# Optimization experiments

Hardware: AMD Instinct MI355X
Metric: run time of the kernel (lower is better)

The kernel has to match this reference:

```python
import jax, jax.numpy as jnp
import numpy as np

K_SIZE = 7
D_MODEL = 128
D_Q = 64
N_HEADS = 4
D_FF = 512
EPS = 1e-5


def _windows(x, k):
    # x: [N,E,H,W] -> [N,E,P,H,W]; zero-padded local k x k windows,
    # row-major over (dy,dx), matching nn.Unfold ordering.
    p = k // 2
    N, E, H, W = x.shape
    xp = jnp.pad(x, ((0, 0), (0, 0), (p, p), (p, p)))
    ws = [xp[:, :, i:i + H, j:j + W] for i in range(k) for j in range(k)]
    return jnp.stack(ws, axis=2)


def _layernorm(x, g, b):
    m = jnp.mean(x, -1, keepdims=True)
    v = jnp.var(x, -1, keepdims=True)
    return (x - m) * jax.lax.rsqrt(v + EPS) * g + b


def setup_inputs() -> dict:
    key = jax.random.key(0)
    ks = jax.random.split(key, 12)
    E, Q, F = D_MODEL, D_Q, D_FF

    def g(k, shape, s=0.02):
        return jax.random.normal(k, shape, jnp.float32) * s

    return dict(
        x=jax.random.normal(ks[0], (4, E, 64, 64), jnp.float32),
        qcoeff=jax.random.normal(ks[1], (4, Q), jnp.float32),
        wq=g(ks[2], (E, E)), bq=jnp.zeros((E,), jnp.float32),
        wk=g(ks[3], (E, E)), bk=jnp.zeros((E,), jnp.float32),
        wv=g(ks[4], (E, E)), bv=jnp.zeros((E,), jnp.float32),
        rel_bias=jnp.zeros((N_HEADS, K_SIZE * K_SIZE), jnp.float32),
        ln1_g=jnp.ones((E,), jnp.float32), ln1_b=jnp.zeros((E,), jnp.float32),
        bil_w=g(ks[5], (E, E, Q)), bil_b=jnp.zeros((E,), jnp.float32),
        ln2_g=jnp.ones((E,), jnp.float32), ln2_b=jnp.zeros((E,), jnp.float32),
        w1=g(ks[6], (F, E)), b1=jnp.zeros((F,), jnp.float32),
        w2=g(ks[7], (E, F)), b2=jnp.zeros((E,), jnp.float32),
    )


def reference(x, qcoeff, wq, bq, wk, bk, wv, bv, rel_bias, ln1_g, ln1_b,
              bil_w, bil_b, ln2_g, ln2_b, w1, b1, w2, b2):
    N, E, H, W = x.shape
    Nh = N_HEADS
    Hd = E // Nh
    P = K_SIZE * K_SIZE

    x_nhwc = jnp.transpose(x, (0, 2, 3, 1))              # [N,H,W,E]
    xn = _layernorm(x_nhwc, ln1_g, ln1_b)
    xnc = jnp.transpose(xn, (0, 3, 1, 2))                # [N,E,H,W]

    # 1x1-conv projections
    q = jnp.einsum('nchw,oc->nohw', xnc, wq) + bq[None, :, None, None]
    k = jnp.einsum('nchw,oc->nohw', xnc, wk) + bk[None, :, None, None]
    v = jnp.einsum('nchw,oc->nohw', xnc, wv) + bv[None, :, None, None]

    # local windows of K/V: [N,Nh,Hd,P,H,W]
    Kw = _windows(k, K_SIZE).reshape(N, Nh, Hd, P, H, W)
    Vw = _windows(v, K_SIZE).reshape(N, Nh, Hd, P, H, W)
    Qh = q.reshape(N, Nh, Hd, H, W)

    scores = jnp.einsum('nhdyx,nhdpyx->nhpyx', Qh, Kw)
    scores = scores + rel_bias[None, :, :, None, None]
    attn = jax.nn.softmax(scores, axis=2)                # softmax over P
    out = jnp.einsum('nhpyx,nhdpyx->nhdyx', attn, Vw).reshape(N, E, H, W)
    z0 = jnp.transpose(out, (0, 2, 3, 1))                # [N,H,W,E]

    # Bilinear(z0, qcoeff): qcoeff constant per (H,W) -> contract once per batch
    t = jnp.einsum('oiq,nq->noi', bil_w, qcoeff)         # [N,E,E]
    z1 = jnp.einsum('nhwi,noi->nhwo', z0, t) + bil_b

    z2 = z1 + x_nhwc
    z3 = _layernorm(z2, ln2_g, ln2_b)
    h1 = jax.nn.gelu(z3 @ w1.T + b1, approximate=False)  # dropout inactive (eval)
    z4 = h1 @ w2.T + b2 + z2
    return jnp.transpose(z4, (0, 3, 1, 2))               # [N,E,H,W]
```

## Files before the change

### kernel.cpp

```cpp
#include <hip/hip_runtime.h>
#include <cmath>

#define EPS 1e-5f
#define SZ 2097152

typedef __attribute__((ext_vector_type(8))) short short8;
typedef __attribute__((ext_vector_type(4))) float floatx4;

__device__ __forceinline__ float dot4(float4 a, float4 b) {
  return fmaf(a.x, b.x, fmaf(a.y, b.y, fmaf(a.z, b.z, a.w * b.w)));
}

__device__ __forceinline__ short f2bf(float f) {
  union { float f; unsigned u; } v; v.f = f;
  unsigned r = v.u + 0x7fff + ((v.u >> 16) & 1);
  return (short)(r >> 16);
}

#define MFMA16(a, b, c) __builtin_amdgcn_mfma_f32_16x16x32_bf16(a, b, c, 0, 0, 0)

__global__ __launch_bounds__(256) void k_prep(const float* __restrict__ w1,
    const float* __restrict__ w2, const float* __restrict__ wq,
    const float* __restrict__ wk, const float* __restrict__ wv,
    const float* __restrict__ bil_w, const float* __restrict__ qcoeff,
    short* __restrict__ w1bf, short* __restrict__ w2bf,
    short* __restrict__ wqbf, short* __restrict__ wkbf, short* __restrict__ wvbf,
    short* __restrict__ tb) {
  __shared__ float qs[256];
  int tid = threadIdx.x;
  qs[tid] = qcoeff[tid];
  __syncthreads();
  int tid0 = blockIdx.x * 256 + tid;
  int stride = gridDim.x * 256;
  for (int i = tid0; i < 16384; i += stride) {
    int flat = i * 4; int f = flat >> 7, c = flat & 127;
    float4 v = *(const float4*)&w1[flat];
    short t4[4] = {f2bf(v.x), f2bf(v.y), f2bf(v.z), f2bf(v.w)};
    *(uint2*)&w1bf[f * 136 + c] = *(uint2*)t4;
  }
  for (int i = tid0; i < 16384; i += stride) {
    int flat = i * 4; int o = flat >> 9, j = flat & 511;
    int ck = j >> 7, jj = j & 127;
    float4 v = *(const float4*)&w2[flat];
    short t4[4] = {f2bf(v.x), f2bf(v.y), f2bf(v.z), f2bf(v.w)};
    *(uint2*)&w2bf[(ck * 128 + o) * 136 + jj] = *(uint2*)t4;
  }
  for (int i = tid0; i < 4096; i += stride) {
    int flat = i * 4; int o = flat >> 7, c = flat & 127;
    float4 a = *(const float4*)&wq[flat];
    float4 b = *(const float4*)&wk[flat];
    float4 cc = *(const float4*)&wv[flat];
    short ta[4] = {f2bf(a.x), f2bf(a.y), f2bf(a.z), f2bf(a.w)};
    short tb4[4] = {f2bf(b.x), f2bf(b.y), f2bf(b.z), f2bf(b.w)};
    short tc[4] = {f2bf(cc.x), f2bf(cc.y), f2bf(cc.z), f2bf(cc.w)};
    *(uint2*)&wqbf[o * 136 + c] = *(uint2*)ta;
    *(uint2*)&wkbf[o * 136 + c] = *(uint2*)tb4;
    *(uint2*)&wvbf[o * 136 + c] = *(uint2*)tc;
  }
  {
    int flat = tid0;
    const float* wrow = bil_w + (size_t)flat * 64;
    float acc[4] = {0.f, 0.f, 0.f, 0.f};
    for (int qq = 0; qq < 64; qq += 4) {
      float4 w4 = *(const float4*)&wrow[qq];
#pragma unroll
      for (int nn = 0; nn < 4; ++nn) {
        const float* qc = &qs[nn * 64 + qq];
        acc[nn] = fmaf(w4.x, qc[0], fmaf(w4.y, qc[1], fmaf(w4.z, qc[2], fmaf(w4.w, qc[3], acc[nn]))));
      }
    }
    int o = flat >> 7, i = flat & 127;
#pragma unroll
    for (int nn = 0; nn < 4; ++nn) tb[nn * 17408 + o * 136 + i] = f2bf(acc[nn]);
  }
}

__global__ __launch_bounds__(512) void k_qkvln(const float* __restrict__ x,
    const float* __restrict__ g, const float* __restrict__ b,
    const short* __restrict__ wqbf, const short* __restrict__ wkbf,
    const short* __restrict__ wvbf, const float* __restrict__ bq,
    const float* __restrict__ bk, const float* __restrict__ bv,
    float* __restrict__ xnhwc, short* __restrict__ qbf,
    short* __restrict__ kbf, short* __restrict__ vtb) {
  __shared__ float tile[128 * 33];
  __shared__ float mres[32], rres[32];
  __shared__ __align__(16) short xs[32 * 136];
  int tid = threadIdx.x;
  int bid = blockIdx.x;
  int half = bid & 1, ny = bid >> 1;
  int n = ny >> 6, y = ny & 63;
  const float* xb = x + (size_t)n * 524288 + y * 64 + half * 32;
  for (int it = 0; it < 8; ++it) {
    int flat = it * 512 + tid;
    int c = flat >> 5, xpl = flat & 31;
    tile[c * 33 + xpl] = xb[(size_t)c * 4096 + xpl];
  }
  __syncthreads();
  {
    int pxl = tid >> 4, cl = tid & 15;
    float s = 0.f, sq = 0.f;
#pragma unroll
    for (int j = 0; j < 8; ++j) {
      float v = tile[(cl * 8 + j) * 33 + pxl];
      s += v; sq += v * v;
    }
    s += __shfl_xor(s, 1);  sq += __shfl_xor(sq, 1);
    s += __shfl_xor(s, 2);  sq += __shfl_xor(sq, 2);
    s += __shfl_xor(s, 4);  sq += __shfl_xor(sq, 4);
    s += __shfl_xor(s, 8);  sq += __shfl_xor(sq, 8);
    if (cl == 0) {
      float m = s * (1.f / 128.f);
      float var = sq * (1.f / 128.f) - m * m;
      mres[pxl] = m;
      rres[pxl] = rsqrtf(var + EPS);
    }
  }
  __syncthreads();
  size_t rowbase = (size_t)ny * 8192 + half * 4096;
  for (int it = 0; it < 8; ++it) {
    int flat = it * 512 + tid;
    int c = flat & 127, pxl = flat >> 7;
    float v = tile[c * 33 + pxl];
    xnhwc[rowbase + flat] = v;
    xs[pxl * 136 + c] = f2bf((v - mres[pxl]) * rres[pxl] * g[c] + b[c]);
  }
  __syncthreads();
  int w = tid >> 6, lane = tid & 63;
  int quad = lane >> 4, r16 = lane & 15;
  int wm = w & 1, wn = w >> 1;
  int stripl = wm * 16;
  short8 a[4];
#pragma unroll
  for (int kk = 0; kk < 4; ++kk)
    a[kk] = *(const short8*)&xs[(stripl + r16) * 136 + kk * 32 + quad * 8];
  const short* wptr[3] = {wqbf, wkbf, wvbf};
  const float* bptr[3] = {bq, bk, bv};
  for (int m = 0; m < 3; ++m) {
    const short* wp = wptr[m];
    const float* bb = bptr[m];
#pragma unroll
    for (int nt = 0; nt < 2; ++nt) {
      int o0 = wn * 32 + nt * 16;
      floatx4 acc = {0.f, 0.f, 0.f, 0.f};
#pragma unroll
      for (int kk = 0; kk < 4; ++kk) {
        short8 bfr = *(const short8*)&wp[(o0 + r16) * 136 + kk * 32 + quad * 8];
        acc = MFMA16(a[kk], bfr, acc);
      }
      float bv2 = bb[o0 + r16];
      if (m < 2) {
        short* dst = (m == 0) ? qbf : kbf;
#pragma unroll
        for (int r = 0; r < 4; ++r) {
          int pxl = stripl + quad * 4 + r;
          dst[rowbase + pxl * 128 + o0 + r16] = f2bf(acc[r] + bv2);
        }
      } else {
        short t4[4] = {f2bf(acc[0] + bv2), f2bf(acc[1] + bv2),
                       f2bf(acc[2] + bv2), f2bf(acc[3] + bv2)};
        *(uint2*)&vtb[(size_t)(n * 128 + o0 + r16) * 4096 + y * 64 + half * 32 +
                      stripl + quad * 4] = *(uint2*)t4;
      }
    }
  }
}

__global__ __launch_bounds__(256) void k_attn(const short* __restrict__ qbf,
    const short* __restrict__ kbf, const short* __restrict__ vtb,
    const float* __restrict__ rel_bias, float* __restrict__ z0) {
  __shared__ float ssf[4][16 * 50];
  __shared__ __align__(16) short AbB[4][16 * 68];
  __shared__ float biasS[4][52];
  int bid = blockIdx.x;
  int h = bid & 3, y = (bid >> 2) & 63, n = bid >> 8;
  int tid = threadIdx.x;
  int w = tid >> 6, lane = tid & 63;
  int quad = lane >> 4, r16 = lane & 15;
  int strip = w * 16;
  float* ssfw = ssf[w];
  short* Abw = AbB[w];
  float* biasw = biasS[w];
  {
    unsigned* ad = (unsigned*)Abw;
    for (int i = lane; i < 544; i += 64) ad[i] = 0u;
  }
  if (lane < 49) biasw[lane] = rel_bias[h * 49 + lane];
  const short* qrow = qbf + (size_t)n * 524288 + (size_t)y * 64 * 128 + h * 32;
  short8 qf = *(const short8*)&qrow[(strip + r16) * 128 + quad * 8];
  const short* kbp = kbf + (size_t)n * 524288 + h * 32;
#pragma unroll
  for (int r = 0; r < 7; ++r) {
    int yy = y + r - 3;
    bool yok = (unsigned)yy < 64u;
    int yyc = min(max(yy, 0), 63);
#pragma unroll
    for (int t = 0; t < 2; ++t) {
      int xxc = (w + t) * 16 + r16;
      int gx = xxc - 3;
      bool ok = yok && ((unsigned)gx < 64u);
      int gxc = min(max(gx, 0), 63);
      short8 bf = *(const short8*)&kbp[(size_t)(yyc * 64 + gxc) * 128 + quad * 8];
      floatx4 c = MFMA16(qf, bf, ((floatx4){0.f, 0.f, 0.f, 0.f}));
#pragma unroll
      for (int rr = 0; rr < 4; ++rr) {
        int lrow = quad * 4 + rr;
        int dx = xxc - (strip + lrow);
        if ((unsigned)dx < 7u) {
          float val = ok ? c[rr] : 0.f;
          ssfw[lrow * 50 + r * 7 + dx] = val + biasw[r * 7 + dx];
        }
      }
    }
  }
  {
    int lrow = lane >> 2, sub = lane & 3;
    int p0 = sub * 12, cnt = (sub == 3) ? 13 : 12;
    float sv[13];
    float mx = -1e30f;
    for (int pi = 0; pi < cnt; ++pi) { sv[pi] = ssfw[lrow * 50 + p0 + pi]; mx = fmaxf(mx, sv[pi]); }
    mx = fmaxf(mx, __shfl_xor(mx, 1));
    mx = fmaxf(mx, __shfl_xor(mx, 2));
    float sum = 0.f;
    for (int pi = 0; pi < cnt; ++pi) { float e = __expf(sv[pi] - mx); sv[pi] = e; sum += e; }
    sum += __shfl_xor(sum, 1);
    sum += __shfl_xor(sum, 2);
    float inv = 1.f / sum;
    for (int pi = 0; pi < cnt; ++pi) ssfw[lrow * 50 + p0 + pi] = sv[pi] * inv;
  }
  floatx4 oacc[2] = {(floatx4){0.f, 0.f, 0.f, 0.f}, (floatx4){0.f, 0.f, 0.f, 0.f}};
  int kk0 = (w == 3) ? 1 : 0;
  int kk1 = (w == 0) ? 0 : 1;
  int lrow = lane >> 2, sub = lane & 3;
  int pxg = strip + lrow;
  const short* vbp = vtb + (size_t)(n * 128 + h * 32) * 4096;
  for (int r = 0; r < 7; ++r) {
    int yy = y + r - 3;
    bool yok = (unsigned)yy < 64u;
    int yyc = min(max(yy, 0), 63);
    int c0 = pxg + sub - 3;
    if ((unsigned)c0 < 64u) Abw[lrow * 68 + c0] = f2bf(ssfw[lrow * 50 + r * 7 + sub]);
    int c1 = pxg + sub + 1;
    if (sub < 3 && (unsigned)c1 < 64u)
      Abw[lrow * 68 + c1] = f2bf(ssfw[lrow * 50 + r * 7 + sub + 4]);
    for (int kk = kk0; kk <= kk1; ++kk) {
      short8 af = *(const short8*)&Abw[r16 * 68 + kk * 32 + quad * 8];
#pragma unroll
      for (int nt = 0; nt < 2; ++nt) {
        short8 vf = *(const short8*)&vbp[(size_t)(nt * 16 + r16) * 4096 + yyc * 64 + kk * 32 + quad * 8];
        if (!yok) vf = (short8){0, 0, 0, 0, 0, 0, 0, 0};
        oacc[nt] = MFMA16(af, vf, oacc[nt]);
      }
    }
  }
  float* zrow = z0 + (size_t)n * 524288 + (size_t)y * 64 * 128 + h * 32;
#pragma unroll
  for (int nt = 0; nt < 2; ++nt)
#pragma unroll
    for (int rr = 0; rr < 4; ++rr) {
      int px = strip + quad * 4 + rr;
      zrow[px * 128 + nt * 16 + r16] = oacc[nt][rr];
    }
}

__global__ __launch_bounds__(512) void k_tail(const float* __restrict__ z0,
    const short* __restrict__ tb, const float* __restrict__ bil_b,
    const float* __restrict__ xnhwc, const float* __restrict__ g2,
    const float* __restrict__ b2ln, const short* __restrict__ w1bf,
    const float* __restrict__ b1, const short* __restrict__ w2bf,
    const float* __restrict__ b2, float* __restrict__ out) {
  __shared__ __align__(16) char smem[8704 + 8704 + 16896];
  short* z3s = (short*)smem;
  short* h1s = (short*)(smem + 8704);
  float* z2s = (float*)(smem + 17408);
  float* outt = (float*)smem;
  int tid = threadIdx.x;
  int bid = blockIdx.x;
  int half = bid & 1, ny = bid >> 1;
  int n = ny >> 6, y = ny & 63;
  size_t rowbase = (size_t)ny * 8192 + half * 4096;
  for (int it = 0; it < 2; ++it) {
    int flat = (it * 512 + tid) * 4;
    int pxl = flat >> 7, c = flat & 127;
    float4 v = *(const float4*)&z0[rowbase + flat];
    short tmp[4] = {f2bf(v.x), f2bf(v.y), f2bf(v.z), f2bf(v.w)};
    *(uint2*)&z3s[pxl * 136 + c] = *(uint2*)tmp;
  }
  __syncthreads();
  int w = tid >> 6, lane = tid & 63;
  int quad = lane >> 4, r16 = lane & 15;
  int wm = w & 1, wn = w >> 1;
  int stripl = wm * 16;
  {
    const short* tn = tb + (size_t)n * 17408;
    short8 a[4];
#pragma unroll
    for (int kk = 0; kk < 4; ++kk)
      a[kk] = *(const short8*)&z3s[(stripl + r16) * 136 + kk * 32 + quad * 8];
#pragma unroll
    for (int nt = 0; nt < 2; ++nt) {
      int o0 = wn * 32 + nt * 16;
      floatx4 acc = {0.f, 0.f, 0.f, 0.f};
#pragma unroll
      for (int kk = 0; kk < 4; ++kk) {
        short8 bfr = *(const short8*)&tn[(o0 + r16) * 136 + kk * 32 + quad * 8];
        acc = MFMA16(a[kk], bfr, acc);
      }
      float bb = bil_b[o0 + r16];
#pragma unroll
      for (int r = 0; r < 4; ++r) {
        int pxl = stripl + quad * 4 + r;
        z2s[pxl * 132 + o0 + r16] = acc[r] + bb + xnhwc[rowbase + pxl * 128 + o0 + r16];
      }
    }
  }
  __syncthreads();
  {
    int pxl = tid >> 4, cl = tid & 15;
    float4 v0 = *(const float4*)&z2s[pxl * 132 + cl * 8];
    float4 v1 = *(const float4*)&z2s[pxl * 132 + cl * 8 + 4];
    float s = v0.x + v0.y + v0.z + v0.w + v1.x + v1.y + v1.z + v1.w;
    float sq = dot4(v0, v0) + dot4(v1, v1);
    s += __shfl_xor(s, 1);  sq += __shfl_xor(sq, 1);
    s += __shfl_xor(s, 2);  sq += __shfl_xor(sq, 2);
    s += __shfl_xor(s, 4);  sq += __shfl_xor(sq, 4);
    s += __shfl_xor(s, 8);  sq += __shfl_xor(sq, 8);
    float m = s * (1.f / 128.f);
    float var = sq * (1.f / 128.f) - m * m;
    float rr = rsqrtf(var + EPS);
    int c0 = cl * 8;
    short t8[8];
#pragma unroll
    for (int j = 0; j < 8; ++j) {
      float vv = (j < 4) ? (&v0.x)[j] : (&v1.x)[j - 4];
      t8[j] = f2bf((vv - m) * rr * g2[c0 + j] + b2ln[c0 + j]);
    }
    *(uint4*)&z3s[pxl * 136 + c0] = *(uint4*)t8;
  }
  __syncthreads();
  short8 a3[4];
#pragma unroll
  for (int kk = 0; kk < 4; ++kk)
    a3[kk] = *(const short8*)&z3s[(stripl + r16) * 136 + kk * 32 + quad * 8];
  floatx4 zacc[2];
  zacc[0] = (floatx4){0.f, 0.f, 0.f, 0.f};
  zacc[1] = (floatx4){0.f, 0.f, 0.f, 0.f};
  for (int fc = 0; fc < 512; fc += 128) {
#pragma unroll
    for (int nt = 0; nt < 2; ++nt) {
      int f0 = wn * 32 + nt * 16;
      floatx4 acc = {0.f, 0.f, 0.f, 0.f};
#pragma unroll
      for (int kk = 0; kk < 4; ++kk) {
        short8 bfr = *(const short8*)&w1bf[(fc + f0 + r16) * 136 + kk * 32 + quad * 8];
        acc = MFMA16(a3[kk], bfr, acc);
      }
      float bb1 = b1[fc + f0 + r16];
#pragma unroll
      for (int r = 0; r < 4; ++r) {
        float hv = acc[r] + bb1;
        float ge = 0.5f * hv * (1.f + erff(hv * 0.70710678118f));
        h1s[(stripl + quad * 4 + r) * 136 + f0 + r16] = f2bf(ge);
      }
    }
    __syncthreads();
    short8 ah[4];
#pragma unroll
    for (int kk = 0; kk < 4; ++kk)
      ah[kk] = *(const short8*)&h1s[(stripl + r16) * 136 + kk * 32 + quad * 8];
    const short* w2ck = w2bf + (fc >> 7) * 17408;
#pragma unroll
    for (int nt = 0; nt < 2; ++nt) {
      int o0 = wn * 32 + nt * 16;
#pragma unroll
      for (int kk = 0; kk < 4; ++kk) {
        short8 bfr = *(const short8*)&w2ck[(o0 + r16) * 136 + kk * 32 + quad * 8];
        zacc[nt] = MFMA16(ah[kk], bfr, zacc[nt]);
      }
    }
    __syncthreads();
  }
#pragma unroll
  for (int nt = 0; nt < 2; ++nt) {
    int o0 = wn * 32 + nt * 16;
    float bb = b2[o0 + r16];
#pragma unroll
    for (int r = 0; r < 4; ++r) {
      int pxl = stripl + quad * 4 + r;
      outt[(o0 + r16) * 33 + pxl] = zacc[nt][r] + bb + z2s[pxl * 132 + o0 + r16];
    }
  }
  __syncthreads();
  for (int it = 0; it < 8; ++it) {
    int flat = it * 512 + tid;
    int o = flat >> 5, pxl = flat & 31;
    out[(((size_t)(n * 128 + o)) * 64 + y) * 64 + half * 32 + pxl] = outt[o * 33 + pxl];
  }
}

extern "C" void kernel_launch(void* const* d_in, const int* in_sizes, int n_in,
                              void* d_out, int out_size, void* d_ws, size_t ws_size,
                              hipStream_t stream) {
  const float* x        = (const float*)d_in[0];
  const float* qcoeff   = (const float*)d_in[1];
  const float* wq       = (const float*)d_in[2];
  const float* bq       = (const float*)d_in[3];
  const float* wk       = (const float*)d_in[4];
  const float* bk       = (const float*)d_in[5];
  const float* wv       = (const float*)d_in[6];
  const float* bv       = (const float*)d_in[7];
  const float* rel_bias = (const float*)d_in[8];
  const float* ln1_g    = (const float*)d_in[9];
  const float* ln1_b    = (const float*)d_in[10];
  const float* bil_w    = (const float*)d_in[11];
  const float* bil_b    = (const float*)d_in[12];
  const float* ln2_g    = (const float*)d_in[13];
  const float* ln2_b    = (const float*)d_in[14];
  const float* w1       = (const float*)d_in[15];
  const float* b1       = (const float*)d_in[16];
  const float* w2       = (const float*)d_in[17];
  const float* b2       = (const float*)d_in[18];
  float* out = (float*)d_out;

  float* ws = (float*)d_ws;
  float* x_nhwc = ws;
  float* z0     = ws + 1 * SZ;
  short* qbf = (short*)(ws + 2 * SZ);
  short* kbf = qbf + SZ;
  short* vtb = kbf + SZ;
  short* bf     = (short*)(ws + 4 * SZ);
  short* tb     = bf;
  short* w1bf   = bf + 4 * 17408;
  short* w2bf   = w1bf + 512 * 136;
  short* wqbf   = w2bf + 4 * 17408;
  short* wkbf   = wqbf + 17408;
  short* wvbf   = wkbf + 17408;

  k_prep<<<64, 256, 0, stream>>>(w1, w2, wq, wk, wv, bil_w, qcoeff,
                                 w1bf, w2bf, wqbf, wkbf, wvbf, tb);
  k_qkvln<<<512, 512, 0, stream>>>(x, ln1_g, ln1_b, wqbf, wkbf, wvbf,
                                   bq, bk, bv, x_nhwc, qbf, kbf, vtb);
  k_attn<<<1024, 256, 0, stream>>>(qbf, kbf, vtb, rel_bias, z0);
  k_tail<<<512, 512, 0, stream>>>(z0, tb, bil_b, x_nhwc, ln2_g, ln2_b,
                                  w1bf, b1, w2bf, b2, out);
}
```

Baseline: 160.1 us.

## Stage weights in LDS, store attention output as bf16, chunk FFN by 64

The QKV and tail kernels now copy weight tiles (Wq/Wk/Wv, the bilinear matrix, and W1/W2 chunks) into shared memory before the MFMA loops, so each element is read from global memory once per block. The attention output z0 is written as bf16, which halves its traffic, and the tail loads it directly into the LDS operand buffer. The residual x is prefetched into registers. The FFN now loops over 64-wide hidden chunks with a compact W2 slice, and k_prep runs with more blocks and a bounds guard. In exchange there are more __syncthreads per chunk and much larger shared-memory use per block (about 63 KB in k_tail), which may reduce occupancy.

```diff
diff --git a/kernel.cpp b/kernel.cpp
--- a/kernel.cpp
+++ b/kernel.cpp
@@ -57,7 +57,7 @@
     *(uint2*)&wkbf[o * 136 + c] = *(uint2*)tb4;
     *(uint2*)&wvbf[o * 136 + c] = *(uint2*)tc;
   }
-  {
+  if (tid0 < 16384) {
     int flat = tid0;
     const float* wrow = bil_w + (size_t)flat * 64;
     float acc[4] = {0.f, 0.f, 0.f, 0.f};
@@ -85,6 +85,7 @@
   __shared__ float tile[128 * 33];
   __shared__ float mres[32], rres[32];
   __shared__ __align__(16) short xs[32 * 136];
+  __shared__ __align__(16) short ws[128 * 136];
   int tid = threadIdx.x;
   int bid = blockIdx.x;
   int half = bid & 1, ny = bid >> 1;
@@ -136,7 +137,11 @@
   const short* wptr[3] = {wqbf, wkbf, wvbf};
   const float* bptr[3] = {bq, bk, bv};
   for (int m = 0; m < 3; ++m) {
+    __syncthreads();
     const short* wp = wptr[m];
+    for (int i = tid; i < 2176; i += 512)
+      *(short8*)&ws[i * 8] = *(const short8*)&wp[i * 8];
+    __syncthreads();
     const float* bb = bptr[m];
 #pragma unroll
     for (int nt = 0; nt < 2; ++nt) {
@@ -144,7 +149,7 @@
       floatx4 acc = {0.f, 0.f, 0.f, 0.f};
 #pragma unroll
       for (int kk = 0; kk < 4; ++kk) {
-        short8 bfr = *(const short8*)&wp[(o0 + r16) * 136 + kk * 32 + quad * 8];
+        short8 bfr = *(const short8*)&ws[(o0 + r16) * 136 + kk * 32 + quad * 8];
         acc = MFMA16(a[kk], bfr, acc);
       }
       float bv2 = bb[o0 + r16];
@@ -167,7 +172,7 @@
 
 __global__ __launch_bounds__(256) void k_attn(const short* __restrict__ qbf,
     const short* __restrict__ kbf, const short* __restrict__ vtb,
-    const float* __restrict__ rel_bias, float* __restrict__ z0) {
+    const float* __restrict__ rel_bias, short* __restrict__ z0bf) {
   __shared__ float ssf[4][16 * 50];
   __shared__ __align__(16) short AbB[4][16 * 68];
   __shared__ float biasS[4][52];
@@ -185,7 +190,7 @@
     for (int i = lane; i < 544; i += 64) ad[i] = 0u;
   }
   if (lane < 49) biasw[lane] = rel_bias[h * 49 + lane];
-  const short* qrow = qbf + (size_t)n * 524288 + (size_t)y * 64 * 128 + h * 32;
+  const short* qrow = qbf + (size_t)n * 524288 + (size_t)y * 8192 + h * 32;
   short8 qf = *(const short8*)&qrow[(strip + r16) * 128 + quad * 8];
   const short* kbp = kbf + (size_t)n * 524288 + h * 32;
 #pragma unroll
@@ -252,46 +257,54 @@
       }
     }
   }
-  float* zrow = z0 + (size_t)n * 524288 + (size_t)y * 64 * 128 + h * 32;
+  short* zrow = z0bf + (size_t)n * 524288 + (size_t)y * 8192 + h * 32;
 #pragma unroll
   for (int nt = 0; nt < 2; ++nt)
 #pragma unroll
     for (int rr = 0; rr < 4; ++rr) {
       int px = strip + quad * 4 + rr;
-      zrow[px * 128 + nt * 16 + r16] = oacc[nt][rr];
-    }
-}
-
-__global__ __launch_bounds__(512) void k_tail(const float* __restrict__ z0,
+      zrow[px * 128 + nt * 16 + r16] = f2bf(oacc[nt][rr]);
+    }
+}
+
+__global__ __launch_bounds__(512) void k_tail(const short* __restrict__ z0bf,
     const short* __restrict__ tb, const float* __restrict__ bil_b,
     const float* __restrict__ xnhwc, const float* __restrict__ g2,
     const float* __restrict__ b2ln, const short* __restrict__ w1bf,
     const float* __restrict__ b1, const short* __restrict__ w2bf,
     const float* __restrict__ b2, float* __restrict__ out) {
-  __shared__ __align__(16) char smem[8704 + 8704 + 16896];
-  short* z3s = (short*)smem;
-  short* h1s = (short*)(smem + 8704);
-  float* z2s = (float*)(smem + 17408);
+  __shared__ __align__(16) char smem[64768];
+  short* R1s = (short*)smem;
+  short* w2c = (short*)(smem + 17408);
+  short* h1s = (short*)(smem + 34816);
   float* outt = (float*)smem;
+  short* z3s = (short*)(smem + 39168);
+  float* z2s = (float*)(smem + 47872);
   int tid = threadIdx.x;
   int bid = blockIdx.x;
   int half = bid & 1, ny = bid >> 1;
   int n = ny >> 6, y = ny & 63;
   size_t rowbase = (size_t)ny * 8192 + half * 4096;
-  for (int it = 0; it < 2; ++it) {
-    int flat = (it * 512 + tid) * 4;
-    int pxl = flat >> 7, c = flat & 127;
-    float4 v = *(const float4*)&z0[rowbase + flat];
-    short tmp[4] = {f2bf(v.x), f2bf(v.y), f2bf(v.z), f2bf(v.w)};
-    *(uint2*)&z3s[pxl * 136 + c] = *(uint2*)tmp;
-  }
-  __syncthreads();
   int w = tid >> 6, lane = tid & 63;
   int quad = lane >> 4, r16 = lane & 15;
   int wm = w & 1, wn = w >> 1;
   int stripl = wm * 16;
-  {
-    const short* tn = tb + (size_t)n * 17408;
+  float xres[2][4];
+#pragma unroll
+  for (int nt = 0; nt < 2; ++nt)
+#pragma unroll
+    for (int r = 0; r < 4; ++r)
+      xres[nt][r] = xnhwc[rowbase + (stripl + quad * 4 + r) * 128 + wn * 32 + nt * 16 + r16];
+  {
+    int flat = tid * 8;
+    int pxl = flat >> 7, c = flat & 127;
+    *(uint4*)&z3s[pxl * 136 + c] = *(const uint4*)&z0bf[rowbase + flat];
+  }
+  const short* tn = tb + (size_t)n * 17408;
+  for (int i = tid; i < 2176; i += 512)
+    *(short8*)&R1s[i * 8] = *(const short8*)&tn[i * 8];
+  __syncthreads();
+  {
     short8 a[4];
 #pragma unroll
     for (int kk = 0; kk < 4; ++kk)
@@ -302,14 +315,14 @@
       floatx4 acc = {0.f, 0.f, 0.f, 0.f};
 #pragma unroll
       for (int kk = 0; kk < 4; ++kk) {
-        short8 bfr = *(const short8*)&tn[(o0 + r16) * 136 + kk * 32 + quad * 8];
+        short8 bfr = *(const short8*)&R1s[(o0 + r16) * 136 + kk * 32 + quad * 8];
         acc = MFMA16(a[kk], bfr, acc);
       }
       float bb = bil_b[o0 + r16];
 #pragma unroll
       for (int r = 0; r < 4; ++r) {
         int pxl = stripl + quad * 4 + r;
-        z2s[pxl * 132 + o0 + r16] = acc[r] + bb + xnhwc[rowbase + pxl * 128 + o0 + r16];
+        z2s[pxl * 132 + o0 + r16] = acc[r] + bb + xres[nt][r];
       }
     }
   }
@@ -344,14 +357,25 @@
   floatx4 zacc[2];
   zacc[0] = (floatx4){0.f, 0.f, 0.f, 0.f};
   zacc[1] = (floatx4){0.f, 0.f, 0.f, 0.f};
-  for (int fc = 0; fc < 512; fc += 128) {
-#pragma unroll
-    for (int nt = 0; nt < 2; ++nt) {
-      int f0 = wn * 32 + nt * 16;
+  for (int fc = 0; fc < 512; fc += 64) {
+    __syncthreads();
+    const short* w1src = w1bf + fc * 136;
+    for (int i = tid; i < 1088; i += 512)
+      *(short8*)&R1s[i * 8] = *(const short8*)&w1src[i * 8];
+    {
+      const short* w2src = w2bf + (fc >> 7) * 17408 + (fc & 127);
+      for (int i = tid; i < 2048; i += 512) {
+        int o = i >> 4, jb = (i & 15) * 4;
+        *(uint2*)&w2c[o * 68 + jb] = *(const uint2*)&w2src[o * 136 + jb];
+      }
+    }
+    __syncthreads();
+    {
+      int f0 = wn * 16;
       floatx4 acc = {0.f, 0.f, 0.f, 0.f};
 #pragma unroll
       for (int kk = 0; kk < 4; ++kk) {
-        short8 bfr = *(const short8*)&w1bf[(fc + f0 + r16) * 136 + kk * 32 + quad * 8];
+        short8 bfr = *(const short8*)&R1s[(f0 + r16) * 136 + kk * 32 + quad * 8];
         acc = MFMA16(a3[kk], bfr, acc);
       }
       float bb1 = b1[fc + f0 + r16];
@@ -359,26 +383,25 @@
       for (int r = 0; r < 4; ++r) {
         float hv = acc[r] + bb1;
         float ge = 0.5f * hv * (1.f + erff(hv * 0.70710678118f));
-        h1s[(stripl + quad * 4 + r) * 136 + f0 + r16] = f2bf(ge);
+        h1s[(stripl + quad * 4 + r) * 68 + f0 + r16] = f2bf(ge);
       }
     }
     __syncthreads();
-    short8 ah[4];
-#pragma unroll
-    for (int kk = 0; kk < 4; ++kk)
-      ah[kk] = *(const short8*)&h1s[(stripl + r16) * 136 + kk * 32 + quad * 8];
-    const short* w2ck = w2bf + (fc >> 7) * 17408;
+    short8 ah[2];
+#pragma unroll
+    for (int kk = 0; kk < 2; ++kk)
+      ah[kk] = *(const short8*)&h1s[(stripl + r16) * 68 + kk * 32 + quad * 8];
 #pragma unroll
     for (int nt = 0; nt < 2; ++nt) {
       int o0 = wn * 32 + nt * 16;
 #pragma unroll
-      for (int kk = 0; kk < 4; ++kk) {
-        short8 bfr = *(const short8*)&w2ck[(o0 + r16) * 136 + kk * 32 + quad * 8];
+      for (int kk = 0; kk < 2; ++kk) {
+        short8 bfr = *(const short8*)&w2c[(o0 + r16) * 68 + kk * 32 + quad * 8];
         zacc[nt] = MFMA16(ah[kk], bfr, zacc[nt]);
       }
     }
-    __syncthreads();
-  }
+  }
+  __syncthreads();
 #pragma unroll
   for (int nt = 0; nt < 2; ++nt) {
     int o0 = wn * 32 + nt * 16;
@@ -423,7 +446,7 @@
 
   float* ws = (float*)d_ws;
   float* x_nhwc = ws;
-  float* z0     = ws + 1 * SZ;
+  short* z0bf   = (short*)(ws + 1 * SZ);
   short* qbf = (short*)(ws + 2 * SZ);
   short* kbf = qbf + SZ;
   short* vtb = kbf + SZ;
@@ -435,11 +458,11 @@
   short* wkbf   = wqbf + 17408;
   short* wvbf   = wkbf + 17408;
 
-  k_prep<<<64, 256, 0, stream>>>(w1, w2, wq, wk, wv, bil_w, qcoeff,
-                                 w1bf, w2bf, wqbf, wkbf, wvbf, tb);
+  k_prep<<<256, 256, 0, stream>>>(w1, w2, wq, wk, wv, bil_w, qcoeff,
+                                  w1bf, w2bf, wqbf, wkbf, wvbf, tb);
   k_qkvln<<<512, 512, 0, stream>>>(x, ln1_g, ln1_b, wqbf, wkbf, wvbf,
                                    bq, bk, bv, x_nhwc, qbf, kbf, vtb);
-  k_attn<<<1024, 256, 0, stream>>>(qbf, kbf, vtb, rel_bias, z0);
-  k_tail<<<512, 512, 0, stream>>>(z0, tb, bil_b, x_nhwc, ln2_g, ln2_b,
+  k_attn<<<1024, 256, 0, stream>>>(qbf, kbf, vtb, rel_bias, z0bf);
+  k_tail<<<512, 512, 0, stream>>>(z0bf, tb, bil_b, x_nhwc, ln2_g, ln2_b,
                                   w1bf, b1, w2bf, b2, out);
 }
```

Result: slower. 177.8 us (+11.0%).
